# Optimization experiments

Measured on AMD Instinct MI355X. Metric: run time of the kernel, lower is better.

The kernel has to match this reference:

```python
import jax, jax.numpy as jnp
import numpy as np
from jax import lax


def ternarize(w):
    # TWN-style ternarization: threshold delta = 0.7*mean|w|, scale alpha =
    # mean |w| over surviving entries; straight-through in backward.
    aw = jnp.abs(w)
    delta = 0.7 * jnp.mean(aw)
    mask = (aw > delta).astype(w.dtype)
    alpha = jnp.sum(aw * mask) / jnp.maximum(jnp.sum(mask), 1.0)
    q = alpha * jnp.sign(w) * mask
    return w + lax.stop_gradient(q - w)


def conv2d(x, w, b):
    # x: [N,C,H,W], w: [O,I,kh,kw]
    y = lax.conv_general_dilated(x, w, window_strides=(1, 1), padding='VALID',
                                 dimension_numbers=('NCHW', 'OIHW', 'NCHW'))
    return y + b[None, :, None, None]


def maxpool2(x):
    return lax.reduce_window(x, -jnp.inf, lax.max,
                             window_dimensions=(1, 1, 2, 2),
                             window_strides=(1, 1, 2, 2), padding='VALID')


def setup_inputs() -> dict:
    key = jax.random.key(0)
    ks = jax.random.split(key, 11)
    n_classes = 10
    x = jax.random.normal(ks[0], (1024, 1, 32, 32), dtype=jnp.float32)
    # Kaiming-ish scaled params
    w1 = jax.random.normal(ks[1], (32, 1, 5, 5), jnp.float32) * (1.0 / np.sqrt(1 * 25))
    b1 = jnp.zeros((32,), jnp.float32)
    w2 = jax.random.normal(ks[2], (64, 32, 5, 5), jnp.float32) * (1.0 / np.sqrt(32 * 25))
    b2 = jnp.zeros((64,), jnp.float32)
    w3 = jax.random.normal(ks[3], (120, 64, 5, 5), jnp.float32) * (1.0 / np.sqrt(64 * 25))
    b3 = jnp.zeros((120,), jnp.float32)
    fw1 = jax.random.normal(ks[4], (84, 120), jnp.float32) * (1.0 / np.sqrt(120))
    fb1 = jnp.zeros((84,), jnp.float32)
    fw2 = jax.random.normal(ks[5], (n_classes, 84), jnp.float32) * (1.0 / np.sqrt(84))
    fb2 = jnp.zeros((n_classes,), jnp.float32)
    return {"x": x, "w1": w1, "b1": b1, "w2": w2, "b2": b2,
            "w3": w3, "b3": b3, "fw1": fw1, "fb1": fb1, "fw2": fw2, "fb2": fb2}


def reference(x, w1, b1, w2, b2, w3, b3, fw1, fb1, fw2, fb2):
    h = jnp.tanh(conv2d(x, ternarize(w1), b1))   # [N,32,28,28]
    h = maxpool2(h)                              # [N,32,14,14]
    h = jnp.tanh(conv2d(h, ternarize(w2), b2))   # [N,64,10,10]
    h = maxpool2(h)                              # [N,64,5,5]
    h = jnp.tanh(conv2d(h, ternarize(w3), b3))   # [N,120,1,1]
    h = h.reshape(h.shape[0], -1)                # [N,120]
    h = jnp.tanh(h @ ternarize(fw1).T + fb1)     # [N,84]
    logits = h @ ternarize(fw2).T + fb2          # [N,n_classes]
    probs = jax.nn.softmax(logits, axis=1)
    return (logits, probs)
```

## Files before the change

### kernel.cpp

```cpp
#include <hip/hip_runtime.h>
#include <hip/hip_bf16.h>
#include <math.h>


typedef __attribute__((ext_vector_type(8))) short bf16x8;
typedef __attribute__((ext_vector_type(4))) float f32x4;

static const size_t OFF_PB    = 0;
static const size_t OFF_W1B   = 256;
static const size_t OFF_W2B   = 1056;
static const size_t OFF_W3B   = 26656;
static const size_t OFF_FW1T  = 129056;
static const size_t OFF_FW2T  = 139136;
static const size_t OFF_P2B   = 139976;
static const size_t OFF_H3    = 959176;

#define BPT 16

__device__ __forceinline__ ushort f2bf(float v) {
    unsigned u = __float_as_uint(v);
    unsigned r = (u + 0x7FFFu + ((u >> 16) & 1u)) >> 16;
    return (ushort)r;
}
__device__ __forceinline__ float bf2f(ushort h) {
    return __uint_as_float((unsigned)h << 16);
}

__device__ __forceinline__ float tanh_fast(float x) {
    float e = __expf(-2.0f * fabsf(x));
    float r = 1.0f - 2.0f * e / (1.0f + e);
    return copysignf(r, x);
}

__device__ __forceinline__ void tensor_select(int tensor,
        const float* w1, const float* w2, const float* w3,
        const float* fw1, const float* fw2,
        const float*& src, int& O, int& K) {
    switch (tensor) {
        case 0: src = w1;  O = 32;  K = 25;   break;
        case 1: src = w2;  O = 64;  K = 800;  break;
        case 2: src = w3;  O = 120; K = 1600; break;
        case 3: src = fw1; O = 84;  K = 120;  break;
        default: src = fw2; O = 10; K = 84;   break;
    }
}

__device__ __forceinline__ float block_sum_256(float v, float* sbuf) {
    #pragma unroll
    for (int off = 32; off > 0; off >>= 1) v += __shfl_down(v, off);
    const int wid = threadIdx.x >> 6;
    if ((threadIdx.x & 63) == 0) sbuf[wid] = v;
    __syncthreads();
    return sbuf[0] + sbuf[1] + sbuf[2] + sbuf[3];
}

__device__ __forceinline__ float alpha_of(const float* pb, int tensor) {
    float s1 = 0.f, c = 0.f;
    #pragma unroll
    for (int i = 0; i < BPT; ++i) {
        s1 += pb[80 + tensor * BPT + i];
        c  += pb[160 + tensor * BPT + i];
    }
    return s1 / fmaxf(c, 1.0f);
}

__global__ __launch_bounds__(256)
void tern_pass1(const float* w1, const float* w2, const float* w3,
                const float* fw1, const float* fw2, float* pb) {
    __shared__ float sbuf[4];
    const int tensor = blockIdx.x / BPT;
    const int blk    = blockIdx.x % BPT;
    const float* src; int O, K;
    tensor_select(tensor, w1, w2, w3, fw1, fw2, src, O, K);
    const int n = O * K;
    float s = 0.f;
    for (int i = blk * 256 + threadIdx.x; i < n; i += BPT * 256)
        s += fabsf(src[i]);
    s = block_sum_256(s, sbuf);
    if (threadIdx.x == 0) pb[tensor * BPT + blk] = s;
}

__global__ __launch_bounds__(256)
void tern_pass2(const float* w1, const float* w2, const float* w3,
                const float* fw1, const float* fw2,
                ushort* w1b, ushort* w2b, ushort* w3b,
                float* fw1t, float* fw2t, float* pb) {
    __shared__ float sbuf[4];
    const int tensor = blockIdx.x / BPT;
    const int blk    = blockIdx.x % BPT;
    const float* src; int O, K;
    tensor_select(tensor, w1, w2, w3, fw1, fw2, src, O, K);
    const int n = O * K;
    float tot = 0.f;
    #pragma unroll
    for (int i = 0; i < BPT; ++i) tot += pb[tensor * BPT + i];
    const float delta = 0.7f * tot / (float)n;

    const ushort BP = 0x3F80u, BN = 0xBF80u;
    float s1 = 0.f, cnt = 0.f;

    if (tensor == 0) {
        for (int j = blk * 256 + threadIdx.x; j < 1024; j += BPT * 256) {
            const int oc = j >> 5, kk = j & 31;
            ushort qb = 0;
            if (kk < 25) {
                float w = src[oc * 25 + kk];
                float aw = fabsf(w);
                if (aw > delta) { s1 += aw; cnt += 1.f; qb = (w > 0.f) ? BP : BN; }
            }
            w1b[j] = qb;
        }
    } else if (tensor == 2) {
        for (int i = blk * 256 + threadIdx.x; i < 128 * 1600; i += BPT * 256) {
            ushort qb = 0;
            if (i < n) {
                float w = src[i];
                float aw = fabsf(w);
                if (aw > delta) { s1 += aw; cnt += 1.f; qb = (w > 0.f) ? BP : BN; }
            }
            w3b[i] = qb;
        }
    } else if (tensor == 1) {
        for (int i = blk * 256 + threadIdx.x; i < n; i += BPT * 256) {
            float w = src[i];
            float aw = fabsf(w);
            ushort qb = 0;
            if (aw > delta) { s1 += aw; cnt += 1.f; qb = (w > 0.f) ? BP : BN; }
            int oc = i / 800;
            int r  = i - oc * 800;
            int ic = r / 25;
            int tap = r - ic * 25;
            w2b[oc * 800 + tap * 32 + ic] = qb;
        }
    } else {
        float* dst = (tensor == 3) ? fw1t : fw2t;
        for (int i = blk * 256 + threadIdx.x; i < n; i += BPT * 256) {
            float w = src[i];
            float aw = fabsf(w);
            float q = 0.f;
            if (aw > delta) { s1 += aw; cnt += 1.f; q = (w > 0.f) ? 1.f : -1.f; }
            int o = i / K;
            int k = i - o * K;
            dst[k * O + o] = q;
        }
    }
    s1 = block_sum_256(s1, sbuf);
    __syncthreads();
    cnt = block_sum_256(cnt, sbuf);
    if (threadIdx.x == 0) {
        pb[80 + tensor * BPT + blk]  = s1;
        pb[160 + tensor * BPT + blk] = cnt;
    }
}

__device__ __forceinline__ void conv2_all(
        const ushort* __restrict__ w2b, const ushort* sxt,
        int n0, int mt0, int lane, f32x4 acc[4][2]) {
    const int col = lane & 15, quad = lane >> 4;
    const ushort* abase[4];
    #pragma unroll
    for (int mi = 0; mi < 4; ++mi) {
        int m = (mt0 + mi) * 16 + col;
        m = m < 100 ? m : 99;
        const int oh = m / 10, ow = m - oh * 10;
        abase[mi] = sxt + (oh * 14 + ow) * 40 + quad * 8;
    }
    const ushort* wb0 = w2b + (size_t)(n0 + col) * 25 * 32 + quad * 8;
    const ushort* wb1 = wb0 + 16 * 25 * 32;
    #pragma unroll
    for (int tap = 0; tap < 25; ++tap) {
        const int kh = tap / 5, kw = tap - kh * 5;
        const int aoff = (kh * 14 + kw) * 40;
        bf16x8 b0 = *(const bf16x8*)(wb0 + tap * 32);
        bf16x8 b1 = *(const bf16x8*)(wb1 + tap * 32);
        #pragma unroll
        for (int mi = 0; mi < 4; ++mi) {
            bf16x8 af = *(const bf16x8*)(abase[mi] + aoff);
            acc[mi][0] = __builtin_amdgcn_mfma_f32_16x16x32_bf16(af, b0, acc[mi][0], 0, 0, 0);
            acc[mi][1] = __builtin_amdgcn_mfma_f32_16x16x32_bf16(af, b1, acc[mi][1], 0, 0, 0);
        }
    }
}

__global__ __launch_bounds__(256)
void conv12_kernel(const float* __restrict__ x, const ushort* __restrict__ w1b,
                   const float* __restrict__ b1, const ushort* __restrict__ w2b,
                   const float* __restrict__ b2, const float* __restrict__ pb,
                   ushort* __restrict__ p2b) {
    __shared__ __align__(16) char smem[40776];
    ushort* A      = (ushort*)smem;
    ushort* sxt    = (ushort*)smem;
    ushort* hb1    = (ushort*)(smem + 15680);
    float*  hb2    = (float*) (smem + 15680);
    ushort* sxb    = (ushort*)(smem + 38720);
    float*  salpha = (float*) (smem + 40768);

    const int n = blockIdx.x;
    const int t = threadIdx.x;
    const int wave = t >> 6, lane = t & 63;
    const int col = lane & 15, quad = lane >> 4;

    bf16x8 B0 = *(const bf16x8*)(w1b + col * 32 + quad * 8);
    bf16x8 B1 = *(const bf16x8*)(w1b + (col + 16) * 32 + quad * 8);

    {
        float4 v = ((const float4*)(x + (size_t)n * 1024))[t];
        ushort4 q;
        q.x = f2bf(v.x); q.y = f2bf(v.y); q.z = f2bf(v.z); q.w = f2bf(v.w);
        *(ushort4*)(sxb + t * 4) = q;
        if (t == 0) salpha[0] = alpha_of(pb, 0);
        if (t == 1) salpha[1] = alpha_of(pb, 1);
    }
    __syncthreads();

    #pragma unroll
    for (int c = 0; c < 4; ++c) {
        const int tbase = c * 13;
        const int ct    = (c == 3) ? 10 : 13;
        const int pbase = tbase * 16;
        const int rows  = ct * 16;

        for (int r = t; r < rows; r += 256) {
            const int p = pbase + r;
            const int oh = p / 28, ow = p % 28;
            ushort v[25];
            #pragma unroll
            for (int kh = 0; kh < 5; ++kh) {
                const ushort* rr = sxb + (oh + kh) * 32 + ow;
                v[kh*5+0]=rr[0]; v[kh*5+1]=rr[1]; v[kh*5+2]=rr[2];
                v[kh*5+3]=rr[3]; v[kh*5+4]=rr[4];
            }
            uint2* arow = (uint2*)(A + r * 36);
            #pragma unroll
            for (int j = 0; j < 6; ++j) {
                uint2 w;
                w.x = (unsigned)v[4*j]   | ((unsigned)v[4*j+1] << 16);
                w.y = (unsigned)v[4*j+2] | ((unsigned)v[4*j+3] << 16);
                arow[j] = w;
            }
            uint2 w6; w6.x = (unsigned)v[24]; w6.y = 0u;
            arow[6] = w6;
            uint2 w7; w7.x = 0u; w7.y = 0u;
            arow[7] = w7;
        }
        __syncthreads();

        for (int tl = wave; tl < ct; tl += 4) {
            const ushort* ap = A + (tl * 16 + col) * 36 + quad * 8;
            ushort4 lo = *(const ushort4*)ap;
            ushort4 hi = *(const ushort4*)(ap + 4);
            bf16x8 af;
            af[0]=(short)lo.x; af[1]=(short)lo.y; af[2]=(short)lo.z; af[3]=(short)lo.w;
            af[4]=(short)hi.x; af[5]=(short)hi.y; af[6]=(short)hi.z; af[7]=(short)hi.w;
            f32x4 z = {};
            f32x4 c0 = __builtin_amdgcn_mfma_f32_16x16x32_bf16(af, B0, z, 0, 0, 0);
            f32x4 c1 = __builtin_amdgcn_mfma_f32_16x16x32_bf16(af, B1, z, 0, 0, 0);
            const int p = pbase + tl * 16 + quad * 4;
            const int oh = p / 28, ow2 = (p % 28) >> 1;
            const int pos = oh * 14 + ow2;
            hb1[pos * 32 + col]            = f2bf(fmaxf(c0[0], c0[1]));
            hb1[(pos + 1) * 32 + col]      = f2bf(fmaxf(c0[2], c0[3]));
            hb1[pos * 32 + col + 16]       = f2bf(fmaxf(c1[0], c1[1]));
            hb1[(pos + 1) * 32 + col + 16] = f2bf(fmaxf(c1[2], c1[3]));
        }
        __syncthreads();
    }

    {
        const float a1 = salpha[0];
        const int oc2 = (t & 15) * 2;
        const float b1a = b1[oc2], b1b = b1[oc2 + 1];
        for (int idx = t; idx < 3136; idx += 256) {
            const int pos2 = idx >> 4;
            const int ph = pos2 / 14, pw = pos2 - ph * 14;
            const int in0 = (2 * ph) * 14 + pw;
            const uint u0 = *(const uint*)(hb1 + in0 * 32 + oc2);
            const uint u1 = *(const uint*)(hb1 + (in0 + 14) * 32 + oc2);
            const float m0 = fmaxf(bf2f((ushort)u0), bf2f((ushort)u1));
            const float m1 = fmaxf(bf2f((ushort)(u0 >> 16)), bf2f((ushort)(u1 >> 16)));
            const ushort r0 = f2bf(tanh_fast(fmaf(a1, m0, b1a)));
            const ushort r1 = f2bf(tanh_fast(fmaf(a1, m1, b1b)));
            *(uint*)(sxt + pos2 * 40 + oc2) = (uint)r0 | ((uint)r1 << 16);
        }
    }
    __syncthreads();

    const int n0  = (wave & 1) * 32;
    const int mt0 = (wave >> 1) * 4;
    f32x4 acc2[4][2] = {};
    conv2_all(w2b, sxt, n0, mt0, lane, acc2);

    {
        #pragma unroll
        for (int mi = 0; mi < 4; ++mi) {
            const int mrow = (mt0 + mi) * 16 + quad * 4;
            if (mrow < 100) {
                #pragma unroll
                for (int np = 0; np < 2; ++np) {
                    const int oc = n0 + np * 16 + col;
                    float2 hm;
                    hm.x = fmaxf(acc2[mi][np][0], acc2[mi][np][1]);
                    hm.y = fmaxf(acc2[mi][np][2], acc2[mi][np][3]);
                    *(float2*)(&hb2[oc * 50 + (mrow >> 1)]) = hm;
                }
            }
        }
    }
    __syncthreads();

    const float a2 = salpha[1];
    for (int idx = t; idx < 1600; idx += 256) {
        const int oc = idx / 25, r = idx - oc * 25;
        const int ph = r / 5, pw = r - ph * 5;
        const float* hb = &hb2[oc * 50 + ph * 10 + pw];
        float m = fmaxf(hb[0], hb[5]);
        p2b[(size_t)n * 1600 + idx] = f2bf(tanh_fast(fmaf(a2, m, b2[oc])));
    }
}

template<int STEPS>
__device__ __forceinline__ void conv3_chunk(const ushort* Abase, const ushort* B0,
                                            f32x4& acc0) {
    #pragma unroll
    for (int s = 0; s < STEPS; ++s) {
        bf16x8 af = *(const bf16x8*)(Abase + s * 32);
        bf16x8 b0 = *(const bf16x8*)(B0 + s * 32);
        acc0 = __builtin_amdgcn_mfma_f32_16x16x32_bf16(af, b0, acc0, 0, 0, 0);
    }
}

__global__ __launch_bounds__(256)
void conv3_mfma(const ushort* __restrict__ p2b, const ushort* __restrict__ w3b,
                const float* __restrict__ b3, const float* __restrict__ pb,
                float* __restrict__ h3) {
    __shared__ float red[4][64][4];
    __shared__ float salpha;
    const int t = threadIdx.x;
    const int wave = t >> 6, lane = t & 63;
    const int mt   = blockIdx.x >> 3;
    const int noct = blockIdx.x & 7;
    const int col = lane & 15, quad = lane >> 4;
    const int kstart = (wave < 2) ? wave * 13 : 26 + (wave - 2) * 12;

    if (t == 0) salpha = alpha_of(pb, 2);

    const ushort* Abase = p2b + (size_t)(mt * 16 + col) * 1600 + kstart * 32 + quad * 8;
    const ushort* B0 = w3b + (size_t)(noct * 16 + col) * 1600 + kstart * 32 + quad * 8;

    f32x4 acc0 = {};
    if (wave < 2) conv3_chunk<13>(Abase, B0, acc0);
    else          conv3_chunk<12>(Abase, B0, acc0);

    #pragma unroll
    for (int r = 0; r < 4; ++r) red[wave][lane][r] = acc0[r];
    __syncthreads();

    {
        const float a3 = salpha;
        const int l = t & 63, vh = t >> 6;
        const int lcol = l & 15, lquad = l >> 4;
        const int img = mt * 16 + lquad * 4 + vh;
        float s = red[0][l][vh] + red[1][l][vh] + red[2][l][vh] + red[3][l][vh];
        const int oc = noct * 16 + lcol;
        if (oc < 120) h3[(size_t)img * 120 + oc] = tanh_fast(fmaf(a3, s, b3[oc]));
    }
}

__global__ __launch_bounds__(128)
void fc_kernel(const float* __restrict__ h3, const float* __restrict__ fw1t,
               const float* __restrict__ fb1, const float* __restrict__ fw2t,
               const float* __restrict__ fb2, const float* __restrict__ pb,
               float* __restrict__ out) {
    const int n = blockIdx.x;
    __shared__ float sh[120];
    __shared__ float sh4[84];
    __shared__ float sl[10];
    __shared__ float salpha[2];
    const int t = threadIdx.x;
    if (t < 120) sh[t] = h3[(size_t)n * 120 + t];
    if (t == 120) salpha[0] = alpha_of(pb, 3);
    if (t == 121) salpha[1] = alpha_of(pb, 4);
    __syncthreads();
    if (t < 84) {
        const float af1 = salpha[0];
        float a = 0.f;
        #pragma unroll 4
        for (int k = 0; k < 120; ++k) a = fmaf(fw1t[k * 84 + t], sh[k], a);
        sh4[t] = tanh_fast(fmaf(af1, a, fb1[t]));
    }
    __syncthreads();
    if (t < 10) {
        const float af2 = salpha[1];
        float a = 0.f;
        #pragma unroll 4
        for (int k = 0; k < 84; ++k) a = fmaf(fw2t[k * 10 + t], sh4[k], a);
        const float lg = fmaf(af2, a, fb2[t]);
        sl[t] = lg;
        out[(size_t)n * 10 + t] = lg;
    }
    __syncthreads();
    if (t < 10) {
        float m = -INFINITY;
        #pragma unroll
        for (int i = 0; i < 10; ++i) m = fmaxf(m, sl[i]);
        float s = 0.f;
        #pragma unroll
        for (int i = 0; i < 10; ++i) s += expf(sl[i] - m);
        out[10240 + (size_t)n * 10 + t] = expf(sl[t] - m) / s;
    }
}

extern "C" void kernel_launch(void* const* d_in, const int* in_sizes, int n_in,
                              void* d_out, int out_size, void* d_ws, size_t ws_size,
                              hipStream_t stream) {
    const float* x   = (const float*)d_in[0];
    const float* w1  = (const float*)d_in[1];
    const float* b1  = (const float*)d_in[2];
    const float* w2  = (const float*)d_in[3];
    const float* b2  = (const float*)d_in[4];
    const float* w3  = (const float*)d_in[5];
    const float* b3  = (const float*)d_in[6];
    const float* fw1 = (const float*)d_in[7];
    const float* fb1 = (const float*)d_in[8];
    const float* fw2 = (const float*)d_in[9];
    const float* fb2 = (const float*)d_in[10];

    float* ws = (float*)d_ws;
    float*  pb   = ws + OFF_PB;
    ushort* w1b  = (ushort*)(ws + OFF_W1B);
    ushort* w2b  = (ushort*)(ws + OFF_W2B);
    ushort* w3b  = (ushort*)(ws + OFF_W3B);
    float*  fw1t = ws + OFF_FW1T;
    float*  fw2t = ws + OFF_FW2T;
    ushort* p2b  = (ushort*)(ws + OFF_P2B);
    float*  h3   = ws + OFF_H3;
    float*  out  = (float*)d_out;

    tern_pass1<<<5 * BPT, 256, 0, stream>>>(w1, w2, w3, fw1, fw2, pb);
    tern_pass2<<<5 * BPT, 256, 0, stream>>>(w1, w2, w3, fw1, fw2,
                                            w1b, w2b, w3b, fw1t, fw2t, pb);
    conv12_kernel<<<1024, 256, 0, stream>>>(x, w1b, b1, w2b, b2, pb, p2b);
    conv3_mfma<<<512, 256, 0, stream>>>(p2b, w3b, b3, pb, h3);
    fc_kernel<<<1024, 128, 0, stream>>>(h3, fw1t, fb1, fw2t, fb2, pb, out);
}
```

Measured before the change: 154.8 us.

## Prefetch conv2 weights into registers and stage FC weights through LDS

In conv2, the B-operand weight fragments are now loaded several taps ahead into a small register ring, so global-load latency overlaps the MFMA work. The conv12 kernel gains a min-blocks-per-CU launch bound, which constrains register allocation. The FC kernel copies fw1 into double-buffered shared memory in chunks with coalesced float4 loads, and copies fw2 into shared memory, replacing strided per-thread global reads. The cost is more registers in conv2, with a risk of spills under the new bound, plus extra LDS and barriers in the FC kernel.

```diff
diff --git a/kernel.cpp b/kernel.cpp
--- a/kernel.cpp
+++ b/kernel.cpp
@@ -153,6 +153,7 @@
     }
 }
 
+#define C2PF 4
 __device__ __forceinline__ void conv2_all(
         const ushort* __restrict__ w2b, const ushort* sxt,
         int n0, int mt0, int lane, f32x4 acc[4][2]) {
@@ -165,14 +166,25 @@
         const int oh = m / 10, ow = m - oh * 10;
         abase[mi] = sxt + (oh * 14 + ow) * 40 + quad * 8;
     }
-    const ushort* wb0 = w2b + (size_t)(n0 + col) * 25 * 32 + quad * 8;
-    const ushort* wb1 = wb0 + 16 * 25 * 32;
+    const ushort* wb0 = w2b + (size_t)(n0 + col) * 800 + quad * 8;
+    const ushort* wb1 = wb0 + 16 * 800;
+    bf16x8 pb0[C2PF], pb1[C2PF];
+    #pragma unroll
+    for (int i = 0; i < C2PF; ++i) {
+        pb0[i] = *(const bf16x8*)(wb0 + i * 32);
+        pb1[i] = *(const bf16x8*)(wb1 + i * 32);
+    }
     #pragma unroll
     for (int tap = 0; tap < 25; ++tap) {
+        const int slot = tap & (C2PF - 1);
+        const bf16x8 b0 = pb0[slot];
+        const bf16x8 b1 = pb1[slot];
+        if (tap + C2PF < 25) {
+            pb0[slot] = *(const bf16x8*)(wb0 + (tap + C2PF) * 32);
+            pb1[slot] = *(const bf16x8*)(wb1 + (tap + C2PF) * 32);
+        }
         const int kh = tap / 5, kw = tap - kh * 5;
         const int aoff = (kh * 14 + kw) * 40;
-        bf16x8 b0 = *(const bf16x8*)(wb0 + tap * 32);
-        bf16x8 b1 = *(const bf16x8*)(wb1 + tap * 32);
         #pragma unroll
         for (int mi = 0; mi < 4; ++mi) {
             bf16x8 af = *(const bf16x8*)(abase[mi] + aoff);
@@ -182,7 +194,7 @@
     }
 }
 
-__global__ __launch_bounds__(256)
+__global__ __launch_bounds__(256, 4)
 void conv12_kernel(const float* __restrict__ x, const ushort* __restrict__ w1b,
                    const float* __restrict__ b1, const ushort* __restrict__ w2b,
                    const float* __restrict__ b2, const float* __restrict__ pb,
@@ -376,25 +388,45 @@
     __shared__ float sh4[84];
     __shared__ float sl[10];
     __shared__ float salpha[2];
+    __shared__ __align__(16) float wbuf[2][30 * 84];
+    __shared__ __align__(16) float fw2s[84 * 10];
     const int t = threadIdx.x;
     if (t < 120) sh[t] = h3[(size_t)n * 120 + t];
     if (t == 120) salpha[0] = alpha_of(pb, 3);
     if (t == 121) salpha[1] = alpha_of(pb, 4);
-    __syncthreads();
-    if (t < 84) {
-        const float af1 = salpha[0];
-        float a = 0.f;
-        #pragma unroll 4
-        for (int k = 0; k < 120; ++k) a = fmaf(fw1t[k * 84 + t], sh[k], a);
-        sh4[t] = tanh_fast(fmaf(af1, a, fb1[t]));
-    }
+    #pragma unroll
+    for (int i = 0; i < 2; ++i) {
+        const int j = t + i * 128;
+        if (j < 210) ((float4*)fw2s)[j] = ((const float4*)fw2t)[j];
+    }
+    for (int i = t; i < 630; i += 128)
+        ((float4*)wbuf[0])[i] = ((const float4*)fw1t)[i];
+    __syncthreads();
+
+    float a = 0.f;
+    #pragma unroll
+    for (int c = 0; c < 4; ++c) {
+        if (c < 3) {
+            const float4* src = (const float4*)(fw1t + (c + 1) * 2520);
+            float4* dst = (float4*)wbuf[(c + 1) & 1];
+            for (int i = t; i < 630; i += 128) dst[i] = src[i];
+        }
+        if (t < 84) {
+            const float* wc = wbuf[c & 1];
+            #pragma unroll 6
+            for (int kk = 0; kk < 30; ++kk)
+                a = fmaf(wc[kk * 84 + t], sh[30 * c + kk], a);
+        }
+        __syncthreads();
+    }
+    if (t < 84) sh4[t] = tanh_fast(fmaf(salpha[0], a, fb1[t]));
     __syncthreads();
     if (t < 10) {
         const float af2 = salpha[1];
-        float a = 0.f;
+        float a2 = 0.f;
         #pragma unroll 4
-        for (int k = 0; k < 84; ++k) a = fmaf(fw2t[k * 10 + t], sh4[k], a);
-        const float lg = fmaf(af2, a, fb2[t]);
+        for (int k = 0; k < 84; ++k) a2 = fmaf(fw2s[k * 10 + t], sh4[k], a2);
+        const float lg = fmaf(af2, a2, fb2[t]);
         sl[t] = lg;
         out[(size_t)n * 10 + t] = lg;
     }
```

Result: no change. 153.0 us (-1.1%).
